# Optimization experiments

Measured on AMD Instinct MI355X. Metric: run time of the kernel, lower is better.

Reference implementation:

```python
import jax, jax.numpy as jnp
import numpy as np

B, H, W, DIM = 4, 128, 128, 64
HEADS, DH, DR = 8, 64, 16
INNER = HEADS * DH  # 512
HID3 = 3 * DR       # 48, wavelet-MLP in_channels
HIDX = 2 * HID3     # 96, wavelet-MLP hidden


def _conv(x, w, stride=1, pad=0, groups=1):
    return jax.lax.conv_general_dilated(
        x, w, (stride, stride), [(pad, pad), (pad, pad)],
        dimension_numbers=('NCHW', 'OIHW', 'NCHW'), feature_group_count=groups)


def _gelu(x):
    return jax.nn.gelu(x, approximate=False)  # torch nn.GELU default (erf)


def _haar_kernel(C):
    h = np.array([[1., 1.], [1., 1.]]) / 2.
    g = np.array([[1., -1.], [1., -1.]]) / 2.
    ht = np.array([[1., 1.], [-1., -1.]]) / 2.
    gt = np.array([[1., -1.], [-1., 1.]]) / 2.
    k = np.stack([h, g, ht, gt])[:, None]          # [4,1,2,2]
    return jnp.asarray(np.tile(k, (C, 1, 1, 1)), jnp.float32)  # [4C,1,2,2], torch repeat layout


def _l2norm(x):
    return x / jnp.maximum(jnp.linalg.norm(x, axis=-1, keepdims=True), 1e-12)


def _spatial(x, dw, pw, gamma):  # SpitialUnit, x NHWC
    t = x.transpose(0, 3, 1, 2)
    C = t.shape[1]
    y = _conv(t, dw, pad=1, groups=C)
    y = _conv(_gelu(y), pw)
    return (t + gamma * y).transpose(0, 2, 3, 1)


def _fourier(x, al_pw, al_dw, ah_pw, ah_dw, ph_pw, ph_scale):  # FourierUnit, x NHWC
    t = x.transpose(0, 3, 1, 2)
    Bc, C, Hc, Wc = t.shape
    X = jnp.fft.rfft2(t, norm='ortho')
    amp, phase = jnp.abs(X), jnp.angle(X)
    Hf, Wf = amp.shape[-2], amp.shape[-1]
    yy = jnp.linspace(0., 1., Hf)[:, None]
    xx = jnp.linspace(0., 1., Wf)[None, :]
    rr = jnp.sqrt(yy ** 2 + xx ** 2)
    low = jax.nn.sigmoid((0.25 - rr) * 20.0)
    high = 1.0 - low
    a_lo = _conv(_gelu(_conv(amp * low[None, None], al_pw)), al_dw, pad=1, groups=C)
    a_hi = _conv(_gelu(_conv(amp * high[None, None], ah_pw)), ah_dw, pad=1, groups=C)
    amp_out = a_lo + a_hi
    phase_out = phase + ph_scale * _conv(phase, ph_pw)
    Y = jax.lax.complex(amp_out * jnp.cos(phase_out), amp_out * jnp.sin(phase_out))
    out = jnp.fft.irfft2(Y, s=(Hc, Wc), norm='ortho')
    return out.transpose(0, 2, 3, 1)


def _wavelet(x, bn_gamma, bn_beta, mlp_in, mlp_dw, mlp_out, res_scale):  # WaveletUnit, x NHWC (H,W even)
    t = x.transpose(0, 3, 1, 2)
    Bc, C, Hc, Wc = t.shape
    y = _conv(t, _haar_kernel(C), stride=2, groups=C)           # [B,4C,H/2,W/2]
    LL, LH, HL, HH = jnp.split(y, 4, axis=1)                    # torch chunk layout
    high = jnp.concatenate([LH, HL, HH], axis=1)                # [B,3C,H/2,W/2]
    # BatchNorm2d in eval mode: running_mean=0, running_var=1, eps=1e-5
    n = high * (bn_gamma / jnp.sqrt(1.0 + 1e-5))[None, :, None, None] + bn_beta[None, :, None, None]
    m = _conv(n, mlp_in)
    m = _gelu(_conv(m, mlp_dw, pad=1, groups=m.shape[1]))
    m = _conv(m, mlp_out)
    high_enh = high + res_scale * m
    x1, x2, x3 = jnp.split(high_enh, 3, axis=1)
    # IWT: out[..., 2i+p, 2j+q] = [LL, x1; x2, x3][p,q]
    arr = jnp.stack([jnp.stack([LL, x1], -1), jnp.stack([x2, x3], -1)], axis=-2)  # [B,C,h,w,p,q]
    Hh, Wh = LL.shape[-2], LL.shape[-1]
    out = arr.transpose(0, 1, 2, 4, 3, 5).reshape(Bc, C, Hh * 2, Wh * 2)
    return out.transpose(0, 2, 3, 1)


def reference(x_in, Wq, Wk, Wv, Wr, We, qs_dw, qs_pw, qs_gamma,
              al_pw, al_dw, ah_pw, ah_dw, ph_pw, ph_scale,
              bn_gamma, bn_beta, mlp_in, mlp_dw, mlp_out, res_scale,
              rescale, Wproj, bproj):
    b, h, w, c = x_in.shape
    hw = h * w
    heads = rescale.shape[0]
    dh = Wq.shape[1] // heads
    dr = Wr.shape[1]
    x = x_in.reshape(b, hw, c)
    q_inp, k_inp, v_inp = x @ Wq, x @ Wk, x @ Wv
    q_dim = (q_inp @ Wr).reshape(b, h, w, dr)
    k_dim = (k_inp @ Wr).reshape(b, h, w, dr)
    v_dim = (v_inp @ Wr).reshape(b, h, w, dr)
    q_mix = _spatial(q_dim, qs_dw, qs_pw, qs_gamma)
    k_mix = _fourier(k_dim, al_pw, al_dw, ah_pw, ah_dw, ph_pw, ph_scale)
    v_mix = _wavelet(v_dim, bn_gamma, bn_beta, mlp_in, mlp_dw, mlp_out, res_scale)
    q_new = q_mix.reshape(b, hw, dr) @ We
    k_new = k_mix.reshape(b, hw, dr) @ We
    v_new = v_mix.reshape(b, hw, dr) @ We

    def pack(t):  # -> [b, heads, dh, hw]
        return t.reshape(b, hw, heads, dh).transpose(0, 2, 3, 1)

    q, k, v = pack(q_new), pack(k_new), pack(v_new)
    q, k = _l2norm(q), _l2norm(k)                       # normalize over hw
    attn = jnp.einsum('bhdn,bhen->bhde', k, q)          # channel attention [b,H,dh,dh]
    attn = jax.nn.softmax(attn * rescale[None], axis=-1)
    o = jnp.einsum('bhde,bhen->bhdn', attn, v)          # [b,H,dh,hw]
    o = o.transpose(0, 3, 1, 2).reshape(b, hw, heads * dh)
    return (o @ Wproj + bproj).reshape(b, h, w, c)


def setup_inputs() -> dict:
    key = jax.random.key(0)
    ks = jax.random.split(key, 20)

    def nrm(k, shape, s=0.02):
        return jax.random.normal(k, shape, jnp.float32) * s

    return {
        'x_in': jax.random.normal(ks[0], (B, H, W, DIM), jnp.float32),
        'Wq': nrm(ks[1], (DIM, INNER)), 'Wk': nrm(ks[2], (DIM, INNER)), 'Wv': nrm(ks[3], (DIM, INNER)),
        'Wr': nrm(ks[4], (INNER, DR)), 'We': nrm(ks[5], (DR, INNER)),
        'qs_dw': nrm(ks[6], (DR, 1, 3, 3)), 'qs_pw': nrm(ks[7], (DR, DR, 1, 1)),
        'qs_gamma': jnp.zeros((1, DR, 1, 1), jnp.float32),
        'al_pw': nrm(ks[8], (DR, DR, 1, 1)), 'al_dw': nrm(ks[9], (DR, 1, 3, 3)),
        'ah_pw': nrm(ks[10], (DR, DR, 1, 1)), 'ah_dw': nrm(ks[11], (DR, 1, 3, 3)),
        'ph_pw': nrm(ks[12], (DR, DR, 1, 1)), 'ph_scale': jnp.asarray(0.01, jnp.float32),
        'bn_gamma': jnp.ones((HID3,), jnp.float32), 'bn_beta': jnp.zeros((HID3,), jnp.float32),
        'mlp_in': nrm(ks[13], (HIDX, HID3, 1, 1)), 'mlp_dw': nrm(ks[14], (HIDX, 1, 3, 3)),
        'mlp_out': nrm(ks[15], (HID3, HIDX, 1, 1)), 'res_scale': jnp.ones((1,), jnp.float32),
        'rescale': jnp.ones((HEADS, 1, 1), jnp.float32),
        'Wproj': nrm(ks[16], (INNER, DIM)), 'bproj': jnp.zeros((DIM,), jnp.float32),
    }
```

## Files before the change

### kernel.cpp

```cpp
#include <hip/hip_runtime.h>
#include <hip/hip_bf16.h>
#include <math.h>

#define HW 16384

__device__ __forceinline__ float LD(const void* p, long i, int bf){
  return bf ? __bfloat162float(((const __hip_bfloat16*)p)[i]) : ((const float*)p)[i];
}
__device__ __forceinline__ float geluf(float x){ return 0.5f*x*(1.0f + erff(x*0.70710678118654752f)); }
__device__ __forceinline__ int rev7(int i){ return (int)(__brev((unsigned)i)>>25); }

__device__ __forceinline__ void fft128(float* Ar, float* Ai, const float* ct, const float* st,
                                       int lane, float dir){
  #pragma unroll
  for(int len=2; len<=128; len<<=1){
    int half=len>>1;
    int pos = lane & (half-1);
    int i1 = ((lane & ~(half-1))<<1) | pos;
    int i2 = i1 + half;
    int tw = pos * (128/len);
    float wr = ct[tw], wi = dir*st[tw];
    float xr=Ar[i2], xi=Ai[i2];
    float tr = xr*wr - xi*wi;
    float ti = xr*wi + xi*wr;
    float ur=Ar[i1], ui=Ai[i1];
    Ar[i1]=ur+tr; Ai[i1]=ui+ti;
    Ar[i2]=ur-tr; Ai[i2]=ui-ti;
  }
}

#define MAKE_TWP(ct,st) { int tt=threadIdx.x; if(tt<128){ float ang=6.283185307179586f*(float)tt/128.f; float s_,c_; sincosf(ang,&s_,&c_); (ct)[tt]=c_; (st)[tt]=s_; } }

#define OFF_M    0
#define OFF_G    3072
#define OFF_MB   6144
#define OFF_FLAG 10240
#define OFF_QDIM 16384
#define OFF_KDIM (16384 + 1048576)
#define OFF_VDIM (16384 + 2*1048576)
#define OFF_QMIX (16384 + 3*1048576)
#define OFF_KMIX (16384 + 4*1048576)
#define OFF_S    (16384 + 5*1048576)
#define FSZ 532480

__global__ void k_head(const void* Wq, const void* Wk, const void* Wv,
                       const void* Wr, const void* bng, float* ws){
  __shared__ float wr[8192];
  __shared__ float part[256];
  int blk=blockIdx.x, t=threadIdx.x;
  if(blk==48){
    for(int i=3072+t;i<10240;i+=256) ws[i]=0.f;
    if(t==0){
      float v = ((const float*)bng)[0];
      ((int*)ws)[OFF_FLAG] = (v==1.0f) ? 0 : 1;
    }
    return;
  }
  int bf = (((const float*)bng)[0]==1.0f) ? 0 : 1;
  int mat=blk>>4, seg=blk&15;
  const void* Wsrc = mat==0 ? Wq : (mat==1 ? Wk : Wv);
  for(int i=t;i<8192;i+=256) wr[i]=LD(Wr,i,bf);
  __syncthreads();
  int o=t&63, jseg=t>>6;
  int c=seg*4+(o>>4), r=o&15;
  float acc=0.f;
  for(int j=jseg*128;j<jseg*128+128;j++) acc += LD(Wsrc,(long)c*512+j,bf)*wr[j*16+r];
  part[jseg*64+o]=acc;
  __syncthreads();
  if(t<64){
    float s=part[t]+part[64+t]+part[128+t]+part[192+t];
    int cc=seg*4+(t>>4), rr=t&15;
    ws[cc*48 + mat*16 + rr]=s;
  }
}

__global__ void k_dims(const void* x, const float* ws,
                       float* qd, float* kd, float* vd, const int* flg){
  int bf=*flg;
  __shared__ __align__(16) float ms[3072];
  __shared__ __align__(16) float xs[64*130];
  int t=threadIdx.x;
  int b = blockIdx.x>>7;
  int pix0 = (blockIdx.x&127)<<7;
  for(int i=t;i<3072;i+=256) ms[i]=ws[i];
  long base = ((long)b*HW + pix0)*64;
  if(!bf){
    const float4* xp = (const float4*)((const float*)x + base);
    for(int e=t;e<2048;e+=256){
      int px=e>>4, c4=(e&15)<<2;
      float4 v = xp[e];
      xs[(c4  )*130+px]=v.x; xs[(c4+1)*130+px]=v.y;
      xs[(c4+2)*130+px]=v.z; xs[(c4+3)*130+px]=v.w;
    }
  } else {
    const uint4* xp = (const uint4*)((const __hip_bfloat16*)x + base);
    for(int e=t;e<1024;e+=256){
      int px=e>>3, c8=(e&7)<<3;
      uint4 u = xp[e];
      unsigned uu[4]={u.x,u.y,u.z,u.w};
      #pragma unroll
      for(int q=0;q<4;q++){
        xs[(c8+2*q  )*130+px] = __uint_as_float((uu[q]&0xffffu)<<16);
        xs[(c8+2*q+1)*130+px] = __uint_as_float(uu[q]&0xffff0000u);
      }
    }
  }
  __syncthreads();
  int pxg=t>>2, rg=t&3;
  int px0=pxg<<1, r0=rg*12;
  float acc0[12], acc1[12];
  #pragma unroll
  for(int j=0;j<12;j++){ acc0[j]=0.f; acc1[j]=0.f; }
  #pragma unroll 4
  for(int c=0;c<64;c++){
    float2 xv = *(const float2*)&xs[c*130+px0];
    const float4* mp = (const float4*)&ms[c*48+r0];
    float4 m0=mp[0], m1=mp[1], m2=mp[2];
    acc0[0]+=xv.x*m0.x; acc0[1]+=xv.x*m0.y; acc0[2]+=xv.x*m0.z; acc0[3]+=xv.x*m0.w;
    acc0[4]+=xv.x*m1.x; acc0[5]+=xv.x*m1.y; acc0[6]+=xv.x*m1.z; acc0[7]+=xv.x*m1.w;
    acc0[8]+=xv.x*m2.x; acc0[9]+=xv.x*m2.y; acc0[10]+=xv.x*m2.z; acc0[11]+=xv.x*m2.w;
    acc1[0]+=xv.y*m0.x; acc1[1]+=xv.y*m0.y; acc1[2]+=xv.y*m0.z; acc1[3]+=xv.y*m0.w;
    acc1[4]+=xv.y*m1.x; acc1[5]+=xv.y*m1.y; acc1[6]+=xv.y*m1.z; acc1[7]+=xv.y*m1.w;
    acc1[8]+=xv.y*m2.x; acc1[9]+=xv.y*m2.y; acc1[10]+=xv.y*m2.z; acc1[11]+=xv.y*m2.w;
  }
  __syncthreads();
  float* sh = xs;
  #pragma unroll
  for(int j=0;j<12;j++){
    sh[(px0  )*49 + r0+j] = acc0[j];
    sh[(px0+1)*49 + r0+j] = acc1[j];
  }
  __syncthreads();
  long ob = ((long)b*HW + pix0)*16;
  for(int e=t;e<2048;e+=256){
    int px=e>>4, rr=e&15;
    qd[ob+e]=sh[px*49 + rr];
    kd[ob+e]=sh[px*49 + 16 + rr];
    vd[ob+e]=sh[px*49 + 32 + rr];
  }
}

__global__ void k_mix3(const float* qd, float* qm, const void* dw, const void* pw, const void* gamma,
                       const float* kd, float* Rre, float* Rim,
                       const float* vd, float* m96, const void* win, const void* bng, const void* bnb,
                       const int* flg){
  __shared__ float smem[9664];
  int bf=*flg;
  int blk=blockIdx.x, t=threadIdx.x;
  if(blk<256){
    float* tile=smem; float* dws=smem+8704; float* pws=smem+8848; float* gsm=smem+9104;
    int b=blk>>6, y0=(blk&63)<<1;
    for(int i=t;i<144;i+=256) dws[i]=LD(dw,i,bf);
    if(t<256) pws[t]=LD(pw,t,bf);
    if(t<16) gsm[t]=LD(gamma,t,bf);
    for(int i=t;i<8192;i+=256){
      int ry=i>>11, rem=i&2047, xx=rem>>4, ch=rem&15;
      int yy=y0-1+ry;
      tile[(ry*128+xx)*17+ch] = (yy>=0&&yy<128) ? qd[(long)(b*128+yy)*2048 + rem] : 0.f;
    }
    __syncthreads();
    int ty=t>>7, x=t&127;
    float g[16];
    for(int ch=0;ch<16;ch++){
      float acc=0.f;
      for(int p=0;p<3;p++)
        for(int q=0;q<3;q++){
          int xx=x-1+q;
          if(xx>=0&&xx<128) acc += dws[ch*9+p*3+q]*tile[((ty+p)*128+xx)*17+ch];
        }
      g[ch]=geluf(acc);
    }
    long ob = ((long)(b*128+y0+ty)*128 + x)*16;
    for(int c=0;c<16;c++){
      float acc=0.f;
      for(int ch=0;ch<16;ch++) acc += pws[c*16+ch]*g[ch];
      qm[ob+c] = tile[((1+ty)*128+x)*17+c] + gsm[c]*acc;
    }
  } else if(blk<512){
    float* slab=smem; float* outre=smem+4160; float* outim=smem+6272;
    float* Ar=smem+8384; float* Ai=smem+8896; float* ct=smem+9408; float* st=smem+9536;
    int blk2=blk-256;
    int b=blk2>>6, y0=(blk2&63)<<1;
    MAKE_TWP(ct,st);
    long gbase = ((long)(b*128+y0))*2048;
    for(int e=t;e<4096;e+=256){
      int yl=e>>11, rem=e&2047, x=rem>>4, c=rem&15;
      slab[yl*2080 + c*130 + x] = kd[gbase + e];
    }
    __syncthreads();
    int w=t>>6, l=t&63, wb=w<<7;
    for(int li=w; li<32; li+=4){
      int yl=li>>4, c=li&15;
      int sb = yl*2080 + c*130;
      float v0=slab[sb+l], v1=slab[sb+64+l];
      int r0=rev7(l), r1=rev7(64+l);
      Ar[wb+r0]=v0; Ai[wb+r0]=0.f;
      Ar[wb+r1]=v1; Ai[wb+r1]=0.f;
      fft128(Ar+wb, Ai+wb, ct, st, l, -1.f);
      int ob = yl*1056 + c*66;
      outre[ob+l]=Ar[wb+l]; outim[ob+l]=Ai[wb+l];
      if(l==0){ outre[ob+64]=Ar[wb+64]; outim[ob+64]=Ai[wb+64]; }
    }
    __syncthreads();
    long obase = ((long)(b*128+y0))*1040;
    for(int e=t;e<2080;e+=256){
      int yl=e/1040, rem=e%1040, v=rem>>4, c=rem&15;
      Rre[obase+e]=outre[yl*1056 + c*66 + v];
      Rim[obase+e]=outim[yl*1056 + c*66 + v];
    }
  } else {
    float* wi=smem; float* vds=smem+4608; float* ns=smem+5632;
    float* gsm=smem+6400; float* bsm=smem+6448;
    int blk3=blk-512;
    int b = blk3>>8;
    int ij0 = (blk3&255)<<4;
    for(int i=t;i<4608;i+=256){ int cc=i/96, ch=i%96; wi[cc*96+ch]=LD(win,(long)ch*48+cc,bf); }
    if(t<48){ gsm[t]=LD(bng,t,bf)*(1.f/sqrtf(1.f+1e-5f)); bsm[t]=LD(bnb,t,bf); }
    int i0 = ij0>>6, j0 = ij0&63;
    long rb0 = ((long)(b*128 + 2*i0)*128 + 2*j0)*16;
    for(int i=t;i<512;i+=256){ vds[i]=vd[rb0+i]; vds[512+i]=vd[rb0+2048+i]; }
    __syncthreads();
    for(int o=t;o<768;o+=256){
      int p=o/48, cc2=o%48;
      int m=cc2+16, c=m>>2, f=m&3;
      float a =vds[(2*p)*16+c],     bv=vds[(2*p+1)*16+c];
      float cv=vds[512+(2*p)*16+c], dv=vds[512+(2*p+1)*16+c];
      float v;
      if(f==0)      v=(a+bv+cv+dv);
      else if(f==1) v=(a-bv+cv-dv);
      else if(f==2) v=(a+bv-cv-dv);
      else          v=(a-bv-cv+dv);
      ns[o] = v*0.5f*gsm[cc2]+bsm[cc2];
    }
    __syncthreads();
    long ob = ((long)b*4096 + ij0)*96;
    for(int o=t;o<1536;o+=256){
      int p=o/96, ch=o%96;
      float acc=0.f;
      for(int cc=0;cc<48;cc++) acc += wi[cc*96+ch]*ns[p*48+cc];
      m96[ob+o]=acc;
    }
  }
}

__global__ void k_fft_col(const float* Rre, const float* Rim,
                          float* glo, float* ghi, float* pho,
                          const void* alpw, const void* ahpw,
                          const void* phpw, const void* phs, const int* flg){
  __shared__ float sre[2080], sim[2080];
  __shared__ float og[2080], oh[2080], op[2080];
  __shared__ float Ar[512], Ai[512];
  __shared__ float ct[128], st[128];
  __shared__ float wl[256], wh[256], wp[256];
  int t=threadIdx.x;
  int bf=*flg;
  int b = blockIdx.x/65, v = blockIdx.x%65;
  MAKE_TWP(ct,st);
  wl[t]=LD(alpw,t,bf); wh[t]=LD(ahpw,t,bf); wp[t]=LD(phpw,t,bf);
  long ibase = ((long)b*128)*1040 + v*16;
  for(int e=t;e<2048;e+=256){
    int y=e>>4, c=e&15;
    sre[c*130+y]=Rre[ibase + (long)y*1040 + c];
    sim[c*130+y]=Rim[ibase + (long)y*1040 + c];
  }
  __syncthreads();
  int w=t>>6, l=t&63, wb=w<<7;
  const float inv=1.f/128.f;
  for(int c=w; c<16; c+=4){
    int sb=c*130;
    float x0r=sre[sb+l], x0i=sim[sb+l], x1r=sre[sb+64+l], x1i=sim[sb+64+l];
    int r0=rev7(l), r1=rev7(64+l);
    Ar[wb+r0]=x0r; Ai[wb+r0]=x0i;
    Ar[wb+r1]=x1r; Ai[wb+r1]=x1i;
    fft128(Ar+wb, Ai+wb, ct, st, l, -1.f);
    float re0=Ar[wb+l]*inv, im0=Ai[wb+l]*inv;
    float re1=Ar[wb+64+l]*inv, im1=Ai[wb+64+l]*inv;
    sre[sb+l]=sqrtf(re0*re0+im0*im0); sim[sb+l]=atan2f(im0,re0);
    sre[sb+64+l]=sqrtf(re1*re1+im1*im1); sim[sb+64+l]=atan2f(im1,re1);
  }
  __syncthreads();
  {
    int u = t&127, half = t>>7;
    float yy=(float)u/127.f, xx=(float)v/64.f;
    float rr=sqrtf(yy*yy+xx*xx);
    float lo = 1.f/(1.f+expf((rr-0.25f)*20.f));
    float hi = 1.f-lo;
    float av[16], pv[16];
    for(int ch=0;ch<16;ch++){ av[ch]=sre[ch*130+u]; pv[ch]=sim[ch*130+u]; }
    float pscale = LD(phs,0,bf);
    for(int c=half*8;c<half*8+8;c++){
      float al=0.f, ah=0.f, pp=0.f;
      for(int ch=0;ch<16;ch++){
        float a=av[ch];
        al += wl[c*16+ch]*(a*lo);
        ah += wh[c*16+ch]*(a*hi);
        pp += wp[c*16+ch]*pv[ch];
      }
      og[c*130+u]=geluf(al); oh[c*130+u]=geluf(ah); op[c*130+u]=pv[c]+pscale*pp;
    }
  }
  __syncthreads();
  long obase = ((long)b*128)*1040 + v*16;
  for(int e=t;e<2048;e+=256){
    int u=e>>4, c=e&15;
    long o = obase + (long)u*1040 + c;
    glo[o]=og[c*130+u]; ghi[o]=oh[c*130+u]; pho[o]=op[c*130+u];
  }
}

__global__ void k_four_dw(const float* glo, const float* ghi, const float* pho,
                          float* Yre, float* Yim,
                          const void* aldw, const void* ahdw, const int* flg){
  int bf=*flg;
  __shared__ float wl[144], wh[144];
  int t=threadIdx.x;
  if(t<144){wl[t]=LD(aldw,t,bf); wh[t]=LD(ahdw,t,bf);}
  __syncthreads();
  long o = (long)blockIdx.x*256+t;
  int c=(int)(o&15); long r=o>>4; int v=(int)(r%65); long r2=r/65; int u=(int)(r2&127); int b=(int)(r2>>7);
  float acc=0.f;
  for(int dp=0;dp<3;dp++){
    int uu=u-1+dp; if(uu<0||uu>=128) continue;
    for(int dq=0;dq<3;dq++){
      int vv=v-1+dq; if(vv<0||vv>=65) continue;
      long idx=(((long)(b*128+uu))*65+vv)*16+c;
      acc += wl[c*9+dp*3+dq]*glo[idx] + wh[c*9+dp*3+dq]*ghi[idx];
    }
  }
  float pvv = pho[o];
  float s_,c_; sincosf(pvv,&s_,&c_);
  Yre[o]=acc*c_; Yim[o]=acc*s_;
}

__global__ void k_ifft_col(const float* Yre, const float* Yim, float* Zre, float* Zim){
  __shared__ float sre[2080], sim[2080];
  __shared__ float Ar[512], Ai[512];
  __shared__ float ct[128], st[128];
  int t=threadIdx.x;
  int b = blockIdx.x/65, v = blockIdx.x%65;
  MAKE_TWP(ct,st);
  long ibase = ((long)b*128)*1040 + v*16;
  for(int e=t;e<2048;e+=256){
    int u=e>>4, c=e&15;
    sre[c*130+u]=Yre[ibase + (long)u*1040 + c];
    sim[c*130+u]=Yim[ibase + (long)u*1040 + c];
  }
  __syncthreads();
  int w=t>>6, l=t&63, wb=w<<7;
  for(int c=w; c<16; c+=4){
    int sb=c*130;
    float x0r=sre[sb+l], x0i=sim[sb+l], x1r=sre[sb+64+l], x1i=sim[sb+64+l];
    int r0=rev7(l), r1=rev7(64+l);
    Ar[wb+r0]=x0r; Ai[wb+r0]=x0i;
    Ar[wb+r1]=x1r; Ai[wb+r1]=x1i;
    fft128(Ar+wb, Ai+wb, ct, st, l, +1.f);
    sre[sb+l]=Ar[wb+l]; sim[sb+l]=Ai[wb+l];
    sre[sb+64+l]=Ar[wb+64+l]; sim[sb+64+l]=Ai[wb+64+l];
  }
  __syncthreads();
  for(int e=t;e<2048;e+=256){
    int y=e>>4, c=e&15;
    Zre[ibase + (long)y*1040 + c]=sre[c*130+y];
    Zim[ibase + (long)y*1040 + c]=sim[c*130+y];
  }
}

__global__ void k_mix2(const float* Zre, const float* Zim, float* km,
                       const float* m96, float* g96, const void* wdw_, const int* flg){
  __shared__ float smem[9664];
  int blk=blockIdx.x, t=threadIdx.x;
  if(blk<256){
    float* szre=smem; float* szim=smem+2112; float* oslab=smem+4224;
    float* Ar=smem+8384; float* Ai=smem+8896; float* ct=smem+9408; float* st=smem+9536;
    int b = blk>>6, y0 = (blk&63)<<1;
    MAKE_TWP(ct,st);
    long ibase = ((long)(b*128+y0))*1040;
    for(int e=t;e<2080;e+=256){
      int yl=e/1040, rem=e%1040, v=rem>>4, c=rem&15;
      szre[yl*1056 + c*66 + v]=Zre[ibase+e];
      szim[yl*1056 + c*66 + v]=Zim[ibase+e];
    }
    __syncthreads();
    int w=t>>6, l=t&63, wb=w<<7;
    const float inv=1.f/128.f;
    for(int li=w; li<32; li+=4){
      int yl=li>>4, c=li&15;
      int sb = yl*1056 + c*66;
      float zr0 = szre[sb+l];
      float zi0 = (l==0)?0.f:szim[sb+l];
      float zr1, zi1;
      if(l==0){ zr1=szre[sb+64]; zi1=0.f; }
      else    { zr1=szre[sb+64-l]; zi1=-szim[sb+64-l]; }
      int r0=rev7(l), r1=rev7(64+l);
      Ar[wb+r0]=zr0; Ai[wb+r0]=zi0;
      Ar[wb+r1]=zr1; Ai[wb+r1]=zi1;
      fft128(Ar+wb, Ai+wb, ct, st, l, +1.f);
      int ob = yl*2080 + c*130;
      oslab[ob+l]=Ar[wb+l]*inv;
      oslab[ob+64+l]=Ar[wb+64+l]*inv;
    }
    __syncthreads();
    long obase = ((long)(b*128+y0))*2048;
    for(int e=t;e<4096;e+=256){
      int yl=e>>11, rem=e&2047, x=rem>>4, c=rem&15;
      km[obase+e]=oslab[yl*2080 + c*130 + x];
    }
  } else {
    int bf=*flg;
    float* wdw=smem;
    for(int i=t;i<864;i+=256) wdw[i]=LD(wdw_,i,bf);
    __syncthreads();
    int o = (blk-256)*256+t;
    int ch = o%96; int r = o/96; int px = r&4095; int b = r>>12;
    int i = px>>6, j = px&63;
    long mb = (long)b*393216;
    float acc=0.f;
    for(int dp=0;dp<3;dp++){ int ii=i-1+dp; if(ii<0||ii>=64) continue;
      for(int dq=0;dq<3;dq++){ int jj=j-1+dq; if(jj<0||jj>=64) continue;
        acc += wdw[ch*9+dp*3+dq]*m96[mb + (long)(ii*64+jj)*96 + ch]; } }
    g96[o]=geluf(acc);
  }
}

__global__ void k_gram(const float* qm, const float* km, float* G){
  __shared__ float qs[256*16], ks[256*16];
  int b=blockIdx.x>>6; int chunk=blockIdx.x&63;
  int t=threadIdx.x; int r=t>>4, s=t&15;
  long pb=((long)b*HW + chunk*256)*16;
  for(int i=t;i<4096;i+=256){ qs[i]=qm[pb+i]; ks[i]=km[pb+i]; }
  __syncthreads();
  float akq=0.f, akk=0.f, aqq=0.f;
  for(int p=0;p<256;p++){
    float kv=ks[p*16+r], qv=qs[p*16+s];
    akq += kv*qv;
    akk += kv*ks[p*16+s];
    aqq += qs[p*16+r]*qv;
  }
  float* Gb=G + b*768;
  atomicAdd(&Gb[t], akq);
  atomicAdd(&Gb[256+t], akk);
  atomicAdd(&Gb[512+t], aqq);
}

__global__ void k_attn(const float* G, float* Mb, const void* We,
                       const void* Wproj, const void* resc, const int* flg){
  int bf=*flg;
  __shared__ float wes[16*64];
  __shared__ float gkq[256], gkk[256], gqq[256];
  __shared__ float ukq[64*16], ukk[64*16], uqq[64*16];
  __shared__ float nk[64], nq[64];
  __shared__ float A[64*64];
  __shared__ float T[64*16];
  __shared__ float wpj[64*64];
  int b=blockIdx.x>>3, h=blockIdx.x&7;
  int t=threadIdx.x;
  for(int i=t;i<1024;i+=256){ int rr=i>>6, e=i&63; wes[rr*64+e]=LD(We, (long)rr*512 + h*64 + e, bf); }
  gkq[t]=G[b*768+t]; gkk[t]=G[b*768+256+t]; gqq[t]=G[b*768+512+t];
  for(int i=t;i<4096;i+=256){ int d=i>>6, c=i&63; wpj[i]=LD(Wproj,(long)(h*64+d)*64+c,bf); }
  __syncthreads();
  for(int i=t;i<1024;i+=256){
    int d=i>>4, s=i&15;
    float a1=0.f,a2=0.f,a3=0.f;
    for(int rr=0;rr<16;rr++){ float wv=wes[rr*64+d]; a1+=wv*gkq[rr*16+s]; a2+=wv*gkk[rr*16+s]; a3+=wv*gqq[rr*16+s]; }
    ukq[i]=a1; ukk[i]=a2; uqq[i]=a3;
  }
  __syncthreads();
  if(t<64){ float a=0.f; for(int s=0;s<16;s++) a+=ukk[t*16+s]*wes[s*64+t]; nk[t]=fmaxf(sqrtf(a),1e-12f); }
  else if(t<128){ int e=t-64; float a=0.f; for(int s=0;s<16;s++) a+=uqq[e*16+s]*wes[s*64+e]; nq[e]=fmaxf(sqrtf(a),1e-12f); }
  __syncthreads();
  float rsc=LD(resc,h,bf);
  for(int i=t;i<4096;i+=256){
    int d=i>>6, e=i&63;
    float a=0.f; for(int s=0;s<16;s++) a+=ukq[d*16+s]*wes[s*64+e];
    A[i]=a/(nk[d]*nq[e])*rsc;
  }
  __syncthreads();
  if(t<64){
    int d=t; float m=-1e30f;
    for(int e=0;e<64;e++) m=fmaxf(m,A[d*64+e]);
    float sum=0.f;
    for(int e=0;e<64;e++){ float ev=expf(A[d*64+e]-m); A[d*64+e]=ev; sum+=ev; }
    float inv=1.f/sum;
    for(int e=0;e<64;e++) A[d*64+e]*=inv;
  }
  __syncthreads();
  for(int i=t;i<1024;i+=256){
    int d=i>>4, s=i&15;
    float a=0.f; for(int e=0;e<64;e++) a+=A[d*64+e]*wes[s*64+e];
    T[i]=a;
  }
  __syncthreads();
  for(int i=t;i<1024;i+=256){
    int s=i>>6, c=i&63;
    float a=0.f; for(int d=0;d<64;d++) a+=T[d*16+s]*wpj[d*64+c];
    atomicAdd(&Mb[b*1024 + s*64 + c], a);
  }
}

__global__ void k_epi2(const float* g96, const float* vd, const float* Mb_,
                       const void* wout_, const void* rs_, const void* bproj,
                       void* out, const int* flg){
  int bf=*flg;
  __shared__ __align__(16) float sg[32*104];
  __shared__ __align__(16) float swt[48*100];
  __shared__ __align__(16) float smb[1024];
  __shared__ float sbias[64];
  int t=threadIdx.x;
  int b = blockIdx.x>>7;
  int rem = blockIdx.x&127;
  int gi = rem>>1;
  int gj0 = (rem&1)<<5;

  long gb = ((long)b*4096 + gi*64 + gj0)*96;
  for(int e=t;e<3072;e+=256){ int px=e/96, ch=e-px*96; sg[px*104+ch]=g96[gb+e]; }
  for(int e=t;e<4608;e+=256){ int cc=e/96, ch=e-cc*96; swt[cc*100+ch]=LD(wout_, e, bf); }
  for(int i=t;i<1024;i+=256) smb[i]=Mb_[b*1024+i];
  if(t<64) sbias[t]=LD(bproj,t,bf);
  __syncthreads();

  int tpx=t>>4, tcc=t&15;
  int px0=tpx<<1, cc0=tcc*3;
  float a00=0.f,a01=0.f,a02=0.f,a10=0.f,a11=0.f,a12=0.f;
  const float4* g4=(const float4*)sg;
  const float4* w4=(const float4*)swt;
  #pragma unroll 4
  for(int ch4=0; ch4<24; ch4++){
    float4 ga=g4[px0*26+ch4], gbv=g4[(px0+1)*26+ch4];
    float4 w0=w4[cc0*25+ch4], w1=w4[(cc0+1)*25+ch4], w2=w4[(cc0+2)*25+ch4];
    a00 += ga.x*w0.x+ga.y*w0.y+ga.z*w0.z+ga.w*w0.w;
    a01 += ga.x*w1.x+ga.y*w1.y+ga.z*w1.z+ga.w*w1.w;
    a02 += ga.x*w2.x+ga.y*w2.y+ga.z*w2.z+ga.w*w2.w;
    a10 += gbv.x*w0.x+gbv.y*w0.y+gbv.z*w0.z+gbv.w*w0.w;
    a11 += gbv.x*w1.x+gbv.y*w1.y+gbv.z*w1.z+gbv.w*w1.w;
    a12 += gbv.x*w2.x+gbv.y*w2.y+gbv.z*w2.z+gbv.w*w2.w;
  }
  __syncthreads();

  float* she = sg;
  float rs=LD(rs_,0,bf);
  float accv[2][3]={{a00,a01,a02},{a10,a11,a12}};
  #pragma unroll
  for(int i=0;i<2;i++)
    #pragma unroll
    for(int j=0;j<3;j++){
      int pxl=px0+i, cc=cc0+j, gj=gj0+pxl;
      int m=cc+16, c=m>>2, f=m&3;
      long vb=((long)(b*128+2*gi)*128 + 2*gj)*16;
      float a=vd[vb+c], bv=vd[vb+16+c], cv=vd[vb+2048+c], dv=vd[vb+2064+c];
      float hv;
      if(f==0)      hv=(a+bv+cv+dv);
      else if(f==1) hv=(a-bv+cv-dv);
      else if(f==2) hv=(a+bv-cv-dv);
      else          hv=(a-bv-cv+dv);
      she[pxl*64 + 16 + cc] = hv*0.5f + rs*accv[i][j];
    }
  for(int o=t;o<512;o+=256){
    int pxl=o>>4, c16=o&15, gj=gj0+pxl;
    int c=c16>>2, f=c16&3;
    long vb=((long)(b*128+2*gi)*128 + 2*gj)*16;
    float a=vd[vb+c], bv=vd[vb+16+c], cv=vd[vb+2048+c], dv=vd[vb+2064+c];
    float hv;
    if(f==0)      hv=(a+bv+cv+dv);
    else if(f==1) hv=(a-bv+cv-dv);
    else if(f==2) hv=(a+bv-cv-dv);
    else          hv=(a-bv-cv+dv);
    she[pxl*64 + c16] = hv*0.5f;
  }
  __syncthreads();

  int c=t&63, xg=t>>6;
  float mbr[16];
  #pragma unroll
  for(int s=0;s<16;s++) mbr[s]=smb[s*64+c];
  float bb=sbias[c];
  long ob0 = ((long)(b*128+2*gi)*128 + 2*gj0)*64;
  for(int k=0;k<32;k++){
    int o=xg+(k<<2);
    int r=o>>6, xl=o&63;
    int hp=xl>>1, pos=((r&1)<<1)|(xl&1);
    const float4* h4=(const float4*)(she + hp*64 + pos*16);
    float4 h0=h4[0],h1=h4[1],h2=h4[2],h3=h4[3];
    float acc=bb;
    acc += h0.x*mbr[0]+h0.y*mbr[1]+h0.z*mbr[2]+h0.w*mbr[3];
    acc += h1.x*mbr[4]+h1.y*mbr[5]+h1.z*mbr[6]+h1.w*mbr[7];
    acc += h2.x*mbr[8]+h2.y*mbr[9]+h2.z*mbr[10]+h2.w*mbr[11];
    acc += h3.x*mbr[12]+h3.y*mbr[13]+h3.z*mbr[14]+h3.w*mbr[15];
    long oo = ob0 + (long)r*8192 + (long)xl*64 + c;
    if(bf) ((__hip_bfloat16*)out)[oo]=__float2bfloat16(acc);
    else   ((float*)out)[oo]=acc;
  }
}

extern "C" void kernel_launch(void* const* d_in, const int* in_sizes, int n_in,
                              void* d_out, int out_size, void* d_ws, size_t ws_size,
                              hipStream_t stream) {
  const void* x_in   = d_in[0];
  const void* Wq     = d_in[1];
  const void* Wk     = d_in[2];
  const void* Wv     = d_in[3];
  const void* Wr     = d_in[4];
  const void* We     = d_in[5];
  const void* qs_dw  = d_in[6];
  const void* qs_pw  = d_in[7];
  const void* qs_g   = d_in[8];
  const void* al_pw  = d_in[9];
  const void* al_dw  = d_in[10];
  const void* ah_pw  = d_in[11];
  const void* ah_dw  = d_in[12];
  const void* ph_pw  = d_in[13];
  const void* ph_s   = d_in[14];
  const void* bn_g   = d_in[15];
  const void* bn_b   = d_in[16];
  const void* mlp_in = d_in[17];
  const void* mlp_dw = d_in[18];
  const void* mlp_out= d_in[19];
  const void* res_s  = d_in[20];
  const void* rescale= d_in[21];
  const void* Wproj  = d_in[22];
  const void* bproj  = d_in[23];
  float* ws = (float*)d_ws;
  const int* flg = ((const int*)ws) + OFF_FLAG;

  float* FA = ws + OFF_S;
  float* FB = FA + FSZ;
  float* FC = FB + FSZ;
  float* FD = FC + FSZ;
  float* FE = FD + FSZ;
  float* M96 = FE + FSZ;
  float* G96 = ws + OFF_QDIM;

  k_head<<<49,256,0,stream>>>(Wq,Wk,Wv,Wr,bn_g, ws);
  k_dims<<<512,256,0,stream>>>(x_in, ws, ws+OFF_QDIM, ws+OFF_KDIM, ws+OFF_VDIM, flg);
  k_mix3<<<1536,256,0,stream>>>(ws+OFF_QDIM, ws+OFF_QMIX, qs_dw, qs_pw, qs_g,
                                ws+OFF_KDIM, FA, FB,
                                ws+OFF_VDIM, M96, mlp_in, bn_g, bn_b, flg);
  k_fft_col<<<260,256,0,stream>>>(FA, FB, FC, FD, FE, al_pw, ah_pw, ph_pw, ph_s, flg);
  k_four_dw<<<2080,256,0,stream>>>(FC, FD, FE, FA, FB, al_dw, ah_dw, flg);
  k_ifft_col<<<260,256,0,stream>>>(FA, FB, FC, FD);
  k_mix2<<<6400,256,0,stream>>>(FC, FD, ws+OFF_KMIX, M96, G96, mlp_dw, flg);
  k_gram<<<256,256,0,stream>>>(ws+OFF_QMIX, ws+OFF_KMIX, ws+OFF_G);
  k_attn<<<32,256,0,stream>>>(ws+OFF_G, ws+OFF_MB, We, Wproj, rescale, flg);
  k_epi2<<<512,256,0,stream>>>(G96, ws+OFF_VDIM, ws+OFF_MB, mlp_out, res_s, bproj, d_out, flg);
}
```

Baseline: 282.8 us.

## Fuse Gram reduction into inverse-FFT kernel and vectorize mix3 conv and MLP paths

The separate Gram kernel is removed. Each inverse-row-FFT block now accumulates the kq, kk and qq Gram products directly from its shared-memory k slab plus the loaded q rows, then atomically adds them into G. This avoids writing k-mix to global memory, reading it back, and one kernel launch. In k_mix3, the depthwise conv now uses a tap-major weight layout with float2 loads and an 18-float padded tile. The wavelet-MLP branch now handles 32 pixels per block with a transposed, padded weight matrix and 12-channel float4 register tiles per thread, which halves that branch's block count. The risks are more shared-memory bank conflicts on the strided oslab reads in the fused Gram loop and different atomic summation order.

```diff
diff --git a/kernel.cpp b/kernel.cpp
--- a/kernel.cpp
+++ b/kernel.cpp
@@ -144,37 +144,52 @@
                        const float* kd, float* Rre, float* Rim,
                        const float* vd, float* m96, const void* win, const void* bng, const void* bnb,
                        const int* flg){
-  __shared__ float smem[9664];
+  __shared__ __align__(16) float smem[9664];
   int bf=*flg;
   int blk=blockIdx.x, t=threadIdx.x;
   if(blk<256){
-    float* tile=smem; float* dws=smem+8704; float* pws=smem+8848; float* gsm=smem+9104;
+    float* tile=smem;
+    float* dws=smem+9216;
+    float* pws=smem+9360;
+    float* gsm=smem+9616;
     int b=blk>>6, y0=(blk&63)<<1;
-    for(int i=t;i<144;i+=256) dws[i]=LD(dw,i,bf);
+    for(int i=t;i<144;i+=256){ int tap=i>>4, ch=i&15; dws[i]=LD(dw,ch*9+tap,bf); }
     if(t<256) pws[t]=LD(pw,t,bf);
     if(t<16) gsm[t]=LD(gamma,t,bf);
     for(int i=t;i<8192;i+=256){
       int ry=i>>11, rem=i&2047, xx=rem>>4, ch=rem&15;
       int yy=y0-1+ry;
-      tile[(ry*128+xx)*17+ch] = (yy>=0&&yy<128) ? qd[(long)(b*128+yy)*2048 + rem] : 0.f;
+      tile[(ry*128+xx)*18+ch] = (yy>=0&&yy<128) ? qd[(long)(b*128+yy)*2048 + rem] : 0.f;
     }
     __syncthreads();
     int ty=t>>7, x=t&127;
-    float g[16];
-    for(int ch=0;ch<16;ch++){
-      float acc=0.f;
-      for(int p=0;p<3;p++)
-        for(int q=0;q<3;q++){
-          int xx=x-1+q;
-          if(xx>=0&&xx<128) acc += dws[ch*9+p*3+q]*tile[((ty+p)*128+xx)*17+ch];
+    float2 g2[8];
+    #pragma unroll
+    for(int k=0;k<8;k++){ g2[k].x=0.f; g2[k].y=0.f; }
+    for(int p=0;p<3;p++){
+      int row=ty+p;
+      for(int q=0;q<3;q++){
+        int xx=x-1+q;
+        if(xx<0||xx>=128) continue;
+        const float2* tv=(const float2*)&tile[(row*128+xx)*18];
+        const float2* wv=(const float2*)&dws[(p*3+q)*16];
+        #pragma unroll
+        for(int k=0;k<8;k++){
+          float2 tt=tv[k], ww=wv[k];
+          g2[k].x += ww.x*tt.x; g2[k].y += ww.y*tt.y;
         }
-      g[ch]=geluf(acc);
-    }
+      }
+    }
+    float ge[16];
+    #pragma unroll
+    for(int k=0;k<8;k++){ ge[2*k]=geluf(g2[k].x); ge[2*k+1]=geluf(g2[k].y); }
     long ob = ((long)(b*128+y0+ty)*128 + x)*16;
     for(int c=0;c<16;c++){
+      const float2* pv=(const float2*)&pws[c*16];
       float acc=0.f;
-      for(int ch=0;ch<16;ch++) acc += pws[c*16+ch]*g[ch];
-      qm[ob+c] = tile[((1+ty)*128+x)*17+c] + gsm[c]*acc;
+      #pragma unroll
+      for(int k=0;k<8;k++){ float2 pp=pv[k]; acc += pp.x*ge[2*k]+pp.y*ge[2*k+1]; }
+      qm[ob+c] = tile[((1+ty)*128+x)*18+c] + gsm[c]*acc;
     }
   } else if(blk<512){
     float* slab=smem; float* outre=smem+4160; float* outim=smem+6272;
@@ -209,37 +224,53 @@
       Rim[obase+e]=outim[yl*1056 + c*66 + v];
     }
   } else {
-    float* wi=smem; float* vds=smem+4608; float* ns=smem+5632;
-    float* gsm=smem+6400; float* bsm=smem+6448;
+    float* wiT=smem;
+    float* vds=smem+4800;
+    float* ns =smem+6848;
+    float* gsm=smem+8416;
+    float* bsm=smem+8464;
     int blk3=blk-512;
-    int b = blk3>>8;
-    int ij0 = (blk3&255)<<4;
-    for(int i=t;i<4608;i+=256){ int cc=i/96, ch=i%96; wi[cc*96+ch]=LD(win,(long)ch*48+cc,bf); }
+    int b = blk3>>7;
+    int hpbase = (blk3&127)<<5;
+    int i0 = hpbase>>6, j0 = hpbase&63;
+    for(int i=t;i<4608;i+=256){ int ch=i/48, cc=i-ch*48; wiT[cc*100+ch]=LD(win,i,bf); }
     if(t<48){ gsm[t]=LD(bng,t,bf)*(1.f/sqrtf(1.f+1e-5f)); bsm[t]=LD(bnb,t,bf); }
-    int i0 = ij0>>6, j0 = ij0&63;
     long rb0 = ((long)(b*128 + 2*i0)*128 + 2*j0)*16;
-    for(int i=t;i<512;i+=256){ vds[i]=vd[rb0+i]; vds[512+i]=vd[rb0+2048+i]; }
-    __syncthreads();
-    for(int o=t;o<768;o+=256){
-      int p=o/48, cc2=o%48;
-      int m=cc2+16, c=m>>2, f=m&3;
-      float a =vds[(2*p)*16+c],     bv=vds[(2*p+1)*16+c];
-      float cv=vds[512+(2*p)*16+c], dv=vds[512+(2*p+1)*16+c];
+    {
+      const float4* v4a=(const float4*)(vd+rb0);
+      const float4* v4b=(const float4*)(vd+rb0+2048);
+      ((float4*)vds)[t] = v4a[t];
+      ((float4*)(vds+1024))[t] = v4b[t];
+    }
+    __syncthreads();
+    for(int o=t;o<1536;o+=256){
+      int p=o/48, cc=o-p*48;
+      int m=cc+16, c=m>>2, f=m&3;
+      float a =vds[(2*p)*16+c],      bv=vds[(2*p+1)*16+c];
+      float cv=vds[1024+(2*p)*16+c], dvv=vds[1024+(2*p+1)*16+c];
       float v;
-      if(f==0)      v=(a+bv+cv+dv);
-      else if(f==1) v=(a-bv+cv-dv);
-      else if(f==2) v=(a+bv-cv-dv);
-      else          v=(a-bv-cv+dv);
-      ns[o] = v*0.5f*gsm[cc2]+bsm[cc2];
-    }
-    __syncthreads();
-    long ob = ((long)b*4096 + ij0)*96;
-    for(int o=t;o<1536;o+=256){
-      int p=o/96, ch=o%96;
-      float acc=0.f;
-      for(int cc=0;cc<48;cc++) acc += wi[cc*96+ch]*ns[p*48+cc];
-      m96[ob+o]=acc;
-    }
+      if(f==0)      v=(a+bv+cv+dvv);
+      else if(f==1) v=(a-bv+cv-dvv);
+      else if(f==2) v=(a+bv-cv-dvv);
+      else          v=(a-bv-cv+dvv);
+      ns[p*49+cc] = v*0.5f*gsm[cc]+bsm[cc];
+    }
+    __syncthreads();
+    int px=t>>3, chg=t&7;
+    int ch0=chg*12;
+    float4 a0={0,0,0,0}, a1={0,0,0,0}, a2={0,0,0,0};
+    #pragma unroll 4
+    for(int cc=0;cc<48;cc++){
+      float nsv = ns[px*49+cc];
+      const float4* wp = (const float4*)&wiT[cc*100+ch0];
+      float4 w0=wp[0], w1=wp[1], w2=wp[2];
+      a0.x+=nsv*w0.x; a0.y+=nsv*w0.y; a0.z+=nsv*w0.z; a0.w+=nsv*w0.w;
+      a1.x+=nsv*w1.x; a1.y+=nsv*w1.y; a1.z+=nsv*w1.z; a1.w+=nsv*w1.w;
+      a2.x+=nsv*w2.x; a2.y+=nsv*w2.y; a2.z+=nsv*w2.z; a2.w+=nsv*w2.w;
+    }
+    long ob = ((long)b*4096 + hpbase + px)*96 + ch0;
+    float4* mp=(float4*)(m96+ob);
+    mp[0]=a0; mp[1]=a1; mp[2]=a2;
   }
 }
 
@@ -365,8 +396,9 @@
   }
 }
 
-__global__ void k_mix2(const float* Zre, const float* Zim, float* km,
-                       const float* m96, float* g96, const void* wdw_, const int* flg){
+__global__ void k_mix2(const float* Zre, const float* Zim, const float* qm,
+                       const float* m96, float* g96, const void* wdw_,
+                       float* G, const int* flg){
   __shared__ float smem[9664];
   int blk=blockIdx.x, t=threadIdx.x;
   if(blk<256){
@@ -400,11 +432,26 @@
       oslab[ob+64+l]=Ar[wb+64+l]*inv;
     }
     __syncthreads();
-    long obase = ((long)(b*128+y0))*2048;
-    for(int e=t;e<4096;e+=256){
-      int yl=e>>11, rem=e&2047, x=rem>>4, c=rem&15;
-      km[obase+e]=oslab[yl*2080 + c*130 + x];
-    }
+    float* qs = smem;
+    long qbase = ((long)(b*128+y0))*2048;
+    for(int e=t;e<4096;e+=256) qs[e]=qm[qbase+e];
+    __syncthreads();
+    int r=t>>4, s=t&15;
+    float akq=0.f, akk=0.f, aqq=0.f;
+    for(int p=0;p<256;p++){
+      int yl=p>>7, x=p&127;
+      float kr = oslab[yl*2080 + r*130 + x];
+      float ks_ = oslab[yl*2080 + s*130 + x];
+      float qr = qs[p*16+r];
+      float qsv= qs[p*16+s];
+      akq += kr*qsv;
+      akk += kr*ks_;
+      aqq += qr*qsv;
+    }
+    float* Gb=G + b*768;
+    atomicAdd(&Gb[t], akq);
+    atomicAdd(&Gb[256+t], akk);
+    atomicAdd(&Gb[512+t], aqq);
   } else {
     int bf=*flg;
     float* wdw=smem;
@@ -420,26 +467,6 @@
         acc += wdw[ch*9+dp*3+dq]*m96[mb + (long)(ii*64+jj)*96 + ch]; } }
     g96[o]=geluf(acc);
   }
-}
-
-__global__ void k_gram(const float* qm, const float* km, float* G){
-  __shared__ float qs[256*16], ks[256*16];
-  int b=blockIdx.x>>6; int chunk=blockIdx.x&63;
-  int t=threadIdx.x; int r=t>>4, s=t&15;
-  long pb=((long)b*HW + chunk*256)*16;
-  for(int i=t;i<4096;i+=256){ qs[i]=qm[pb+i]; ks[i]=km[pb+i]; }
-  __syncthreads();
-  float akq=0.f, akk=0.f, aqq=0.f;
-  for(int p=0;p<256;p++){
-    float kv=ks[p*16+r], qv=qs[p*16+s];
-    akq += kv*qv;
-    akk += kv*ks[p*16+s];
-    aqq += qs[p*16+r]*qv;
-  }
-  float* Gb=G + b*768;
-  atomicAdd(&Gb[t], akq);
-  atomicAdd(&Gb[256+t], akk);
-  atomicAdd(&Gb[512+t], aqq);
 }
 
 __global__ void k_attn(const float* G, float* Mb, const void* We,
@@ -631,14 +658,13 @@
 
   k_head<<<49,256,0,stream>>>(Wq,Wk,Wv,Wr,bn_g, ws);
   k_dims<<<512,256,0,stream>>>(x_in, ws, ws+OFF_QDIM, ws+OFF_KDIM, ws+OFF_VDIM, flg);
-  k_mix3<<<1536,256,0,stream>>>(ws+OFF_QDIM, ws+OFF_QMIX, qs_dw, qs_pw, qs_g,
+  k_mix3<<<1024,256,0,stream>>>(ws+OFF_QDIM, ws+OFF_QMIX, qs_dw, qs_pw, qs_g,
                                 ws+OFF_KDIM, FA, FB,
                                 ws+OFF_VDIM, M96, mlp_in, bn_g, bn_b, flg);
   k_fft_col<<<260,256,0,stream>>>(FA, FB, FC, FD, FE, al_pw, ah_pw, ph_pw, ph_s, flg);
   k_four_dw<<<2080,256,0,stream>>>(FC, FD, FE, FA, FB, al_dw, ah_dw, flg);
   k_ifft_col<<<260,256,0,stream>>>(FA, FB, FC, FD);
-  k_mix2<<<6400,256,0,stream>>>(FC, FD, ws+OFF_KMIX, M96, G96, mlp_dw, flg);
-  k_gram<<<256,256,0,stream>>>(ws+OFF_QMIX, ws+OFF_KMIX, ws+OFF_G);
+  k_mix2<<<6400,256,0,stream>>>(FC, FD, ws+OFF_QMIX, M96, G96, mlp_dw, ws+OFF_G, flg);
   k_attn<<<32,256,0,stream>>>(ws+OFF_G, ws+OFF_MB, We, Wproj, rescale, flg);
   k_epi2<<<512,256,0,stream>>>(G96, ws+OFF_VDIM, ws+OFF_MB, mlp_out, res_s, bproj, d_out, flg);
 }
```

Result: faster. 271.0 us (-4.2%).
